# Kernel optimization log

Hardware: AMD Instinct MI355X
Metric: run time of the kernel (lower is better)

Reference implementation:

```python
import jax, jax.numpy as jnp
import numpy as np

S, G, NMUL, LENF = 730, 4000, 2, 15
NEARZERO = 1e-5

# param bounds (change_param_range: lb + raw*(ub-lb)), raw in [0,1]
HBV_LB = np.array([1., 50., .05, .01, .001, .2, 0., 0., -2.5, .5, 0., 0.], np.float32)
HBV_UB = np.array([6., 1000., .9, .5, .2, 1., 10., 100., 2.5, 10., .1, .2], np.float32)
EXP_LB = np.array([0., 100., 10., 0., 0., -3.], np.float32)
EXP_UB = np.array([.1, 1500., 50., 5., 3., 0.], np.float32)


def _descale(raw, lb, ub):
    # raw: [G, n_par, NMUL]
    return lb[None, :, None] + raw * (ub - lb)[None, :, None]


def _hbv(P, T, PET, ph):
    # ph: [G,12,NMUL]; order: beta fc k0 k1 k2 lp perc uzl tt cfmax cfr cwh
    beta, fc, k0, k1, k2, lp, perc, uzl, tt, cfmax, cfr, cwh = [ph[:, i, :] for i in range(12)]

    def step(carry, inp):
        sp, mw, sm, suz, slz = carry
        p, t, pet = inp
        rain = jnp.where(t >= tt, p, 0.)
        sp = sp + jnp.where(t < tt, p, 0.)
        melt = jnp.minimum(jnp.maximum(cfmax * (t - tt), 0.), sp)
        mw = mw + melt; sp = sp - melt
        refr = jnp.minimum(jnp.maximum(cfr * cfmax * (tt - t), 0.), mw)
        sp = sp + refr; mw = mw - refr
        tosoil = jnp.maximum(mw - cwh * sp, 0.)
        mw = mw - tosoil
        sw = jnp.clip((sm / fc) ** beta, 0., 1.)
        rech = (rain + tosoil) * sw
        sm = sm + rain + tosoil - rech
        excess = jnp.maximum(sm - fc, 0.); sm = sm - excess
        et = jnp.minimum(pet * jnp.clip(sm / (lp * fc), 0., 1.), sm)
        sm = jnp.maximum(sm - et, NEARZERO)
        suz = suz + rech + excess
        pa = jnp.minimum(perc, suz); suz = suz - pa
        q0 = k0 * jnp.maximum(suz - uzl, 0.); suz = suz - q0
        q1 = k1 * suz; suz = suz - q1
        slz = slz + pa
        q2 = k2 * slz; slz = slz - q2
        return (sp, mw, sm, suz, slz), q0 + q1 + q2

    z = jnp.full_like(fc, NEARZERO)
    init = (z, z, 0.5 * fc, z, z)
    _, q = jax.lax.scan(step, init, (P, T, PET))
    return q  # [S,G,NMUL]


def _exphydro(P, T, PET, pe):
    # pe: [G,6,NMUL]; order: f smax qmax df tmax tmin
    f, smax, qmax, df, tmax, tmin = [pe[:, i, :] for i in range(6)]

    def step(carry, inp):
        s0, s1 = carry
        p, t, pet = inp
        ps = jnp.where(t <= tmin, p, 0.)
        pr = p - ps
        melt = jnp.where(t > tmax, jnp.minimum(s0, df * (t - tmax)), 0.)
        s0 = s0 + ps - melt
        s1 = s1 + pr + melt
        qspill = jnp.maximum(s1 - smax, 0.); s1 = s1 - qspill
        et = jnp.minimum(pet * jnp.clip(s1 / smax, 0., 1.), s1); s1 = s1 - et
        qb = jnp.minimum(qmax * jnp.exp(-f * jnp.maximum(smax - s1, 0.)), s1)
        s1 = s1 - qb
        return (s0, s1), qspill + qb

    z = jnp.full_like(smax, NEARZERO)
    init = (z, 0.5 * smax)
    _, q = jax.lax.scan(step, init, (P, T, PET))
    return q  # [S,G,NMUL]


def _uh_gamma(a, b):
    # a,b: [G]; gamma-pdf unit hydrograph, lenF=LENF
    aa = jax.nn.relu(a) + 0.1
    th = jax.nn.relu(b) + 0.5
    t = jnp.arange(LENF, dtype=jnp.float32) + 0.5  # [LENF]
    logw = (-jax.scipy.special.gammaln(aa)[None, :] - aa[None, :] * jnp.log(th)[None, :]
            + (aa - 1.)[None, :] * jnp.log(t)[:, None] - t[:, None] / th[None, :])
    w = jnp.exp(logw)
    return w / w.sum(0, keepdims=True)  # [LENF,G]


def _route(q, w):
    # causal depthwise conv: out[t,g] = sum_k w[k,g] * q[t-k,g]
    qp = jnp.pad(q, ((LENF - 1, 0), (0, 0)))
    out = jnp.zeros_like(q)
    for k in range(LENF):
        out = out + w[k][None, :] * qp[LENF - 1 - k: LENF - 1 - k + q.shape[0]]
    return out


def setup_inputs() -> dict:
    key = jax.random.key(0)
    k1, k2 = jax.random.split(key)
    u = jax.random.uniform(k1, (S, G, 3), dtype=jnp.float32)
    # physical forcing ranges: prcp [0,10] mm/d, tmean [-10,20] C, pet [0,5] mm/d
    x = jnp.stack([u[..., 0] * 10., u[..., 1] * 30. - 10., u[..., 2] * 5.], axis=-1)
    raw_phy_static = jax.random.uniform(k2, (G, 18 * NMUL + 2), dtype=jnp.float32)
    return {"x": x, "raw_phy_static": raw_phy_static}


def reference(x, raw_phy_static):
    # unpack: [G, 18*NMUL] static block + 2 routing params
    static = raw_phy_static[:, :18 * NMUL].reshape(G, 18, NMUL)
    ph = _descale(static[:, :12, :], jnp.asarray(HBV_LB), jnp.asarray(HBV_UB))
    pe = _descale(static[:, 12:, :], jnp.asarray(EXP_LB), jnp.asarray(EXP_UB))
    route = raw_phy_static[:, 18 * NMUL:]
    rout_a = route[:, 0] * 2.9   # bounds [0, 2.9]
    rout_b = route[:, 1] * 6.5   # bounds [0, 6.5]

    P = jnp.broadcast_to(x[:, :, 0, None], (S, G, NMUL))
    T = jnp.broadcast_to(x[:, :, 1, None], (S, G, NMUL))
    PET = jnp.broadcast_to(x[:, :, 2, None], (S, G, NMUL))

    q_hbv = _hbv(P, T, PET, ph)
    q_exp = _exphydro(P, T, PET, pe)
    qsim = 0.5 * (q_hbv.mean(-1) + q_exp.mean(-1))  # blend over models, mean over nmul -> [S,G]

    w = _uh_gamma(rout_a, rout_b)
    return _route(qsim, w)  # [S,G] routed streamflow
```

## Files before the change

kernel.cpp:

```cpp
#include <hip/hip_runtime.h>

#define SS 730
#define GG 4000
#define LENF 15
#define PD 10
#define GPAD 4032
#define TT 10
#define QN ((size_t)SS * GG)
#define QNI ((int)(SS * GG))

template<bool STORE4>
__global__ __launch_bounds__(64, 1) void hydro_scan(const float* __restrict__ x,
                                                    const float* __restrict__ raw,
                                                    float* __restrict__ qsim) {
    int tid = blockIdx.x * 64 + threadIdx.x;
    int g = tid % GPAD;
    int inst = tid / GPAD;
    if (g >= GG) return;
    int m = inst & 1;
    const float* pr = raw + (size_t)g * 38 + m;

    int xoff = g * 3;
    int qoff = g + (STORE4 ? inst * QNI : 0);

    float pb[PD], tb[PD], eb[PD];
#pragma unroll
    for (int j = 0; j < PD; ++j) {
        pb[j] = x[xoff]; tb[j] = x[xoff + 1]; eb[j] = x[xoff + 2];
        xoff += 3 * GG;
    }

    if (inst < 2) {
        float beta  = 1.0f   + pr[0]  * 5.0f;
        float fc    = 50.0f  + pr[2]  * 950.0f;
        float k0    = 0.05f  + pr[4]  * 0.85f;
        float k1    = 0.01f  + pr[6]  * 0.49f;
        float k2    = 0.001f + pr[8]  * 0.199f;
        float lp    = 0.2f   + pr[10] * 0.8f;
        float perc  =          pr[12] * 10.0f;
        float uzl   =          pr[14] * 100.0f;
        float tt    = -2.5f  + pr[16] * 5.0f;
        float cfmax = 0.5f   + pr[18] * 9.5f;
        float cfr   =          pr[20] * 0.1f;
        float cwh   =          pr[22] * 0.2f;
        float invfc   = 1.0f / fc;
        float invlpfc = 1.0f / (lp * fc);
        float ncfrcf  = -(cfr * cfmax);
        float omk0    = 1.0f - k0;
        float k0uzl   = k0 * uzl;
        float omk1    = 1.0f - k1;

        float sp = 1e-5f, mw = 1e-5f, sm = 0.5f * fc, suz = 1e-5f, slz = 1e-5f;

        auto body = [&](float p, float tc, float pet) -> float {
            float dt   = tc - tt;
            float msn  = fmaxf(cfmax * dt, 0.0f);
            float mrf  = fmaxf(ncfrcf * dt, 0.0f);
            float rain = (dt >= 0.0f) ? p : 0.0f;
            float snow = p - rain;
            float etk  = fmaf(-invlpfc, pet, 1.0f);
            float sw   = exp2f(beta * __log2f(sm * invfc));
            float omsw = 1.0f - sw;
            float sp1  = sp + snow;
            float melt = fminf(msn, sp1);
            float mw2  = mw + melt;
            float sp2  = sp1 - melt;
            float refr = fminf(mrf, mw2);
            float mw3  = mw2 - refr;
            sp = sp2 + refr;
            float mw4  = fminf(mw3, cwh * sp);
            float tosoil = mw3 - mw4;
            mw = mw4;
            float rt    = rain + tosoil;
            float sm1   = fmaf(rt, omsw, sm);
            float rech  = rt * sw;
            float excess = fmaxf(sm1 - fc, 0.0f);
            float sm2   = fminf(sm1, fc);
            sm = fmaxf(fmaxf(sm2 * etk, sm2 - pet), 1e-5f);
            float suz1 = suz + rech + excess;
            float suz2 = fmaxf(suz1 - perc, 0.0f);
            float pa   = suz1 - suz2;
            float suz3 = fminf(suz2, fmaf(suz2, omk0, k0uzl));
            float suzn = omk1 * suz3;
            float q01  = suz2 - suzn;
            suz = suzn;
            float slz1 = slz + pa;
            float q2   = k2 * slz1;
            slz = slz1 - q2;
            return q01 + q2;
        };

        for (int c = 0; c < SS / PD - 1; ++c) {
#pragma unroll
            for (int j = 0; j < PD; ++j) {
                float p = pb[j], tc = tb[j], pet = eb[j];
                pb[j] = x[xoff]; tb[j] = x[xoff + 1]; eb[j] = x[xoff + 2];
                xoff += 3 * GG;
                float q = body(p, tc, pet);
                if (STORE4) qsim[qoff] = q; else atomicAdd(&qsim[qoff], 0.25f * q);
                qoff += GG;
            }
        }
#pragma unroll
        for (int j = 0; j < PD; ++j) {
            float q = body(pb[j], tb[j], eb[j]);
            if (STORE4) qsim[qoff] = q; else atomicAdd(&qsim[qoff], 0.25f * q);
            qoff += GG;
        }
    } else {
        const float* pe = pr + 24;
        float f    =           pe[0]  * 0.1f;
        float smax = 100.0f  + pe[2]  * 1400.0f;
        float qmax = 10.0f   + pe[4]  * 40.0f;
        float df   =           pe[6]  * 5.0f;
        float tmax =           pe[8]  * 3.0f;
        float tmin = -3.0f   + pe[10] * 3.0f;
        float invsmax = 1.0f / smax;
        float fl = f * 1.44269504f;
        float c0 = __log2f(qmax) - fl * smax;

        float s0 = 1e-5f, s1 = 0.5f * smax;

        auto body = [&](float p, float tc, float pet) -> float {
            float mdf = df * fmaxf(tc - tmax, 0.0f);
            float ps  = (tc <= tmin) ? p : 0.0f;
            float prr = p - ps;
            float etk = fmaxf(fmaf(-invsmax, pet, 1.0f), 0.0f);
            float mlt = fminf(s0, mdf);
            s0 = fmaxf(s0 - mdf, 0.0f) + ps;
            float s1a = s1 + prr + mlt;
            float qspill = fmaxf(s1a - smax, 0.0f);
            float s1b = fminf(s1a, smax);
            float s1c = s1b * etk;
            float qb  = fminf(exp2f(fmaf(fl, s1c, c0)), s1c);
            s1 = s1c - qb;
            return qspill + qb;
        };

        for (int c = 0; c < SS / PD - 1; ++c) {
#pragma unroll
            for (int j = 0; j < PD; ++j) {
                float p = pb[j], tc = tb[j], pet = eb[j];
                pb[j] = x[xoff]; tb[j] = x[xoff + 1]; eb[j] = x[xoff + 2];
                xoff += 3 * GG;
                float q = body(p, tc, pet);
                if (STORE4) qsim[qoff] = q; else atomicAdd(&qsim[qoff], 0.25f * q);
                qoff += GG;
            }
        }
#pragma unroll
        for (int j = 0; j < PD; ++j) {
            float q = body(pb[j], tb[j], eb[j]);
            if (STORE4) qsim[qoff] = q; else atomicAdd(&qsim[qoff], 0.25f * q);
            qoff += GG;
        }
    }
}

__global__ __launch_bounds__(256) void uh_weights(const float* __restrict__ raw,
                                                  float* __restrict__ wbuf) {
    int g = blockIdx.x * 256 + threadIdx.x;
    if (g >= GG) return;
    float a = raw[(size_t)g * 38 + 36] * 2.9f;
    float b = raw[(size_t)g * 38 + 37] * 6.5f;
    float aa = fmaxf(a, 0.0f) + 0.1f;
    float th = fmaxf(b, 0.0f) + 0.5f;
    float am1 = aa - 1.0f;
    float invth = 1.0f / th;

    const float logt[LENF] = {
        -0.69314718f, 0.40546511f, 0.91629073f, 1.25276297f, 1.50407740f,
         1.70474809f, 1.87180218f, 2.01490302f, 2.14006616f, 2.25129180f,
         2.35137526f, 2.44234704f, 2.52572864f, 2.60268969f, 2.67414865f };

    float w[LENF];
    float s = 0.0f;
#pragma unroll
    for (int k = 0; k < LENF; ++k) {
        float tk = (float)k + 0.5f;
        w[k] = expf(am1 * logt[k] - tk * invth);
        s += w[k];
    }
    float scale = 0.25f / s;
#pragma unroll
    for (int k = 0; k < LENF; ++k)
        wbuf[(size_t)k * GG + g] = w[k] * scale;
}

template<int NB, bool WPRE>
__global__ __launch_bounds__(256) void hydro_route(const float* __restrict__ qsim,
                                                   const float* __restrict__ raw,
                                                   const float* __restrict__ wbuf,
                                                   float* __restrict__ out) {
    int idx = blockIdx.x * 256 + threadIdx.x;
    if (idx >= GG * (SS / TT)) return;
    int g = idx % GG;
    int c = idx / GG;
    int t0 = c * TT;

    float w[LENF];
    float scale;
    if (WPRE) {
#pragma unroll
        for (int k = 0; k < LENF; ++k)
            w[k] = wbuf[(size_t)k * GG + g];
        scale = 1.0f;
    } else {
        float a = raw[(size_t)g * 38 + 36] * 2.9f;
        float b = raw[(size_t)g * 38 + 37] * 6.5f;
        float aa = fmaxf(a, 0.0f) + 0.1f;
        float th = fmaxf(b, 0.0f) + 0.5f;
        float am1 = aa - 1.0f;
        float invth = 1.0f / th;
        const float logt[LENF] = {
            -0.69314718f, 0.40546511f, 0.91629073f, 1.25276297f, 1.50407740f,
             1.70474809f, 1.87180218f, 2.01490302f, 2.14006616f, 2.25129180f,
             2.35137526f, 2.44234704f, 2.52572864f, 2.60268969f, 2.67414865f };
        float s = 0.0f;
#pragma unroll
        for (int k = 0; k < LENF; ++k) {
            float tk = (float)k + 0.5f;
            w[k] = expf(am1 * logt[k] - tk * invth);
            s += w[k];
        }
        scale = (NB == 4 ? 0.25f : 1.0f) / s;
    }

    float v[TT + LENF - 1];
#pragma unroll
    for (int i = 0; i < TT + LENF - 1; ++i) {
        int tp = t0 - (LENF - 1) + i;
        float sv = 0.0f;
        if (tp >= 0) {
            const float* qb = qsim + (size_t)tp * GG + g;
            sv = qb[0];
            if (NB == 4) sv += qb[QN] + qb[2 * QN] + qb[3 * QN];
        }
        v[i] = sv;
    }
#pragma unroll
    for (int j = 0; j < TT; ++j) {
        float acc = 0.0f;
#pragma unroll
        for (int k = 0; k < LENF; ++k)
            acc += w[k] * v[j + (LENF - 1) - k];
        out[(size_t)(t0 + j) * GG + g] = (WPRE ? acc : acc * scale);
    }
}

extern "C" void kernel_launch(void* const* d_in, const int* in_sizes, int n_in,
                              void* d_out, int out_size, void* d_ws, size_t ws_size,
                              hipStream_t stream) {
    const float* x   = (const float*)d_in[0];
    const float* raw = (const float*)d_in[1];
    float* out  = (float*)d_out;
    float* qsim = (float*)d_ws;

    const size_t slices4 = 4 * QN * sizeof(float);
    const size_t wbytes  = (size_t)LENF * GG * sizeof(float);
    int rblocks = (GG * (SS / TT) + 255) / 256;

    if (ws_size >= slices4 + wbytes) {
        float* wbuf = qsim + 4 * QN;
        hydro_scan<true><<<(4 * GPAD) / 64, 64, 0, stream>>>(x, raw, qsim);
        uh_weights<<<(GG + 255) / 256, 256, 0, stream>>>(raw, wbuf);
        hydro_route<4, true><<<rblocks, 256, 0, stream>>>(qsim, raw, wbuf, out);
    } else if (ws_size >= slices4) {
        hydro_scan<true><<<(4 * GPAD) / 64, 64, 0, stream>>>(x, raw, qsim);
        hydro_route<4, false><<<rblocks, 256, 0, stream>>>(qsim, raw, nullptr, out);
    } else {
        hipMemsetAsync(qsim, 0, QN * sizeof(float), stream);
        hydro_scan<false><<<(4 * GPAD) / 64, 64, 0, stream>>>(x, raw, qsim);
        hydro_route<1, false><<<rblocks, 256, 0, stream>>>(qsim, raw, nullptr, out);
    }
}
```

Baseline: 111.2 us.

## Software-pipeline HBV and ExpHydro recurrences across timesteps to shorten dependency chains

Splits each timestep of both the HBV and ExpHydro scan bodies into stages (snow, soil, response) and skews them across consecutive timesteps. The soil-wetness power term for the next step is computed right after the soil update, so its log/exp latency overlaps with independent work from other stages. The goal is to break the serial latency chain in this latency-bound, one-wave-per-block recurrence. The cost is extra prologue and epilogue code and more live registers, and the launcher drops the middle workspace-size branch.

```diff
diff --git a/kernel.cpp b/kernel.cpp
--- a/kernel.cpp
+++ b/kernel.cpp
@@ -51,16 +51,18 @@
         float omk1    = 1.0f - k1;
 
         float sp = 1e-5f, mw = 1e-5f, sm = 0.5f * fc, suz = 1e-5f, slz = 1e-5f;
-
-        auto body = [&](float p, float tc, float pet) -> float {
+        float swc = exp2f(beta * __log2f(sm * invfc));
+        float rech = 0.0f, exc = 0.0f;
+        float rech_b = 0.0f, exc_b = 0.0f;
+        float rt_p = 0.0f, pet_p = 0.0f;
+        float qprev = 0.0f;
+
+        auto S1 = [&](float p, float tc) -> float {
             float dt   = tc - tt;
             float msn  = fmaxf(cfmax * dt, 0.0f);
             float mrf  = fmaxf(ncfrcf * dt, 0.0f);
             float rain = (dt >= 0.0f) ? p : 0.0f;
             float snow = p - rain;
-            float etk  = fmaf(-invlpfc, pet, 1.0f);
-            float sw   = exp2f(beta * __log2f(sm * invfc));
-            float omsw = 1.0f - sw;
             float sp1  = sp + snow;
             float melt = fminf(msn, sp1);
             float mw2  = mw + melt;
@@ -71,13 +73,20 @@
             float mw4  = fminf(mw3, cwh * sp);
             float tosoil = mw3 - mw4;
             mw = mw4;
-            float rt    = rain + tosoil;
-            float sm1   = fmaf(rt, omsw, sm);
-            float rech  = rt * sw;
-            float excess = fmaxf(sm1 - fc, 0.0f);
-            float sm2   = fminf(sm1, fc);
+            return rain + tosoil;
+        };
+        auto S2 = [&](float rt, float pet) {
+            float omsw = 1.0f - swc;
+            float sm1  = fmaf(rt, omsw, sm);
+            rech = rt * swc;
+            exc  = fmaxf(sm1 - fc, 0.0f);
+            float sm2  = fminf(sm1, fc);
+            float etk  = fmaf(-invlpfc, pet, 1.0f);
             sm = fmaxf(fmaxf(sm2 * etk, sm2 - pet), 1e-5f);
-            float suz1 = suz + rech + excess;
+            swc = exp2f(beta * __log2f(sm * invfc));
+        };
+        auto S3 = [&](float rb, float ebx) -> float {
+            float suz1 = suz + rb + ebx;
             float suz2 = fmaxf(suz1 - perc, 0.0f);
             float pa   = suz1 - suz2;
             float suz3 = fminf(suz2, fmaf(suz2, omk0, k0uzl));
@@ -89,24 +98,57 @@
             slz = slz1 - q2;
             return q01 + q2;
         };
-
-        for (int c = 0; c < SS / PD - 1; ++c) {
-#pragma unroll
-            for (int j = 0; j < PD; ++j) {
-                float p = pb[j], tc = tb[j], pet = eb[j];
+        auto full = [&](int j, bool pre, bool st) {
+            if (st) {
+                if (STORE4) qsim[qoff] = qprev;
+                else atomicAdd(&qsim[qoff], 0.25f * qprev);
+                qoff += GG;
+            }
+            float p = pb[j], tc = tb[j], pet = eb[j];
+            if (pre) {
                 pb[j] = x[xoff]; tb[j] = x[xoff + 1]; eb[j] = x[xoff + 2];
                 xoff += 3 * GG;
-                float q = body(p, tc, pet);
-                if (STORE4) qsim[qoff] = q; else atomicAdd(&qsim[qoff], 0.25f * q);
-                qoff += GG;
             }
-        }
-#pragma unroll
-        for (int j = 0; j < PD; ++j) {
-            float q = body(pb[j], tb[j], eb[j]);
-            if (STORE4) qsim[qoff] = q; else atomicAdd(&qsim[qoff], 0.25f * q);
-            qoff += GG;
-        }
+            float qv = S3(rech_b, exc_b);
+            S2(rt_p, pet_p);
+            float rt = S1(p, tc);
+            rech_b = rech; exc_b = exc;
+            rt_p = rt; pet_p = pet;
+            qprev = qv;
+        };
+
+        {
+            float p = pb[0], tc = tb[0], pet = eb[0];
+            pb[0] = x[xoff]; tb[0] = x[xoff + 1]; eb[0] = x[xoff + 2];
+            xoff += 3 * GG;
+            rt_p = S1(p, tc); pet_p = pet;
+        }
+        {
+            float p = pb[1], tc = tb[1], pet = eb[1];
+            pb[1] = x[xoff]; tb[1] = x[xoff + 1]; eb[1] = x[xoff + 2];
+            xoff += 3 * GG;
+            S2(rt_p, pet_p);
+            rech_b = rech; exc_b = exc;
+            rt_p = S1(p, tc); pet_p = pet;
+        }
+        full(2, true, false);
+#pragma unroll
+        for (int j = 3; j < PD; ++j) full(j, true, true);
+        for (int c = 1; c < SS / PD - 1; ++c) {
+#pragma unroll
+            for (int j = 0; j < PD; ++j) full(j, true, true);
+        }
+#pragma unroll
+        for (int j = 0; j < PD; ++j) full(j, false, true);
+        if (STORE4) { qsim[qoff] = qprev; qoff += GG; }
+        else { atomicAdd(&qsim[qoff], 0.25f * qprev); qoff += GG; }
+        S2(rt_p, pet_p);
+        float qv = S3(rech_b, exc_b);
+        if (STORE4) { qsim[qoff] = qv; qoff += GG; }
+        else { atomicAdd(&qsim[qoff], 0.25f * qv); qoff += GG; }
+        float qf = S3(rech, exc);
+        if (STORE4) qsim[qoff] = qf;
+        else atomicAdd(&qsim[qoff], 0.25f * qf);
     } else {
         const float* pe = pr + 24;
         float f    =           pe[0]  * 0.1f;
@@ -120,14 +162,19 @@
         float c0 = __log2f(qmax) - fl * smax;
 
         float s0 = 1e-5f, s1 = 0.5f * smax;
-
-        auto body = [&](float p, float tc, float pet) -> float {
+        float prr_p = 0.0f, mlt_p = 0.0f, pet_p = 0.0f;
+        float qprev = 0.0f;
+
+        auto S1e = [&](float p, float tc) {
             float mdf = df * fmaxf(tc - tmax, 0.0f);
             float ps  = (tc <= tmin) ? p : 0.0f;
             float prr = p - ps;
-            float etk = fmaxf(fmaf(-invsmax, pet, 1.0f), 0.0f);
             float mlt = fminf(s0, mdf);
             s0 = fmaxf(s0 - mdf, 0.0f) + ps;
+            prr_p = prr; mlt_p = mlt;
+        };
+        auto S2e = [&](float prr, float mlt, float pet) -> float {
+            float etk = fmaxf(fmaf(-invsmax, pet, 1.0f), 0.0f);
             float s1a = s1 + prr + mlt;
             float qspill = fmaxf(s1a - smax, 0.0f);
             float s1b = fminf(s1a, smax);
@@ -136,24 +183,44 @@
             s1 = s1c - qb;
             return qspill + qb;
         };
-
-        for (int c = 0; c < SS / PD - 1; ++c) {
-#pragma unroll
-            for (int j = 0; j < PD; ++j) {
-                float p = pb[j], tc = tb[j], pet = eb[j];
+        auto full = [&](int j, bool pre, bool st) {
+            if (st) {
+                if (STORE4) qsim[qoff] = qprev;
+                else atomicAdd(&qsim[qoff], 0.25f * qprev);
+                qoff += GG;
+            }
+            float p = pb[j], tc = tb[j], pet = eb[j];
+            if (pre) {
                 pb[j] = x[xoff]; tb[j] = x[xoff + 1]; eb[j] = x[xoff + 2];
                 xoff += 3 * GG;
-                float q = body(p, tc, pet);
-                if (STORE4) qsim[qoff] = q; else atomicAdd(&qsim[qoff], 0.25f * q);
-                qoff += GG;
             }
-        }
-#pragma unroll
-        for (int j = 0; j < PD; ++j) {
-            float q = body(pb[j], tb[j], eb[j]);
-            if (STORE4) qsim[qoff] = q; else atomicAdd(&qsim[qoff], 0.25f * q);
-            qoff += GG;
-        }
+            float prr = prr_p, mlt = mlt_p, peto = pet_p;
+            S1e(p, tc);
+            float qv = S2e(prr, mlt, peto);
+            pet_p = pet;
+            qprev = qv;
+        };
+
+        {
+            float p = pb[0], tc = tb[0], pet = eb[0];
+            pb[0] = x[xoff]; tb[0] = x[xoff + 1]; eb[0] = x[xoff + 2];
+            xoff += 3 * GG;
+            S1e(p, tc); pet_p = pet;
+        }
+        full(1, true, false);
+#pragma unroll
+        for (int j = 2; j < PD; ++j) full(j, true, true);
+        for (int c = 1; c < SS / PD - 1; ++c) {
+#pragma unroll
+            for (int j = 0; j < PD; ++j) full(j, true, true);
+        }
+#pragma unroll
+        for (int j = 0; j < PD; ++j) full(j, false, true);
+        if (STORE4) { qsim[qoff] = qprev; qoff += GG; }
+        else { atomicAdd(&qsim[qoff], 0.25f * qprev); qoff += GG; }
+        float qf = S2e(prr_p, mlt_p, pet_p);
+        if (STORE4) qsim[qoff] = qf;
+        else atomicAdd(&qsim[qoff], 0.25f * qf);
     }
 }
 
@@ -259,18 +326,16 @@
     const size_t slices4 = 4 * QN * sizeof(float);
     const size_t wbytes  = (size_t)LENF * GG * sizeof(float);
     int rblocks = (GG * (SS / TT) + 255) / 256;
+    int sblocks = (4 * GPAD) / 64;
 
     if (ws_size >= slices4 + wbytes) {
         float* wbuf = qsim + 4 * QN;
-        hydro_scan<true><<<(4 * GPAD) / 64, 64, 0, stream>>>(x, raw, qsim);
+        hydro_scan<true><<<sblocks, 64, 0, stream>>>(x, raw, qsim);
         uh_weights<<<(GG + 255) / 256, 256, 0, stream>>>(raw, wbuf);
         hydro_route<4, true><<<rblocks, 256, 0, stream>>>(qsim, raw, wbuf, out);
-    } else if (ws_size >= slices4) {
-        hydro_scan<true><<<(4 * GPAD) / 64, 64, 0, stream>>>(x, raw, qsim);
-        hydro_route<4, false><<<rblocks, 256, 0, stream>>>(qsim, raw, nullptr, out);
     } else {
         hipMemsetAsync(qsim, 0, QN * sizeof(float), stream);
-        hydro_scan<false><<<(4 * GPAD) / 64, 64, 0, stream>>>(x, raw, qsim);
+        hydro_scan<false><<<sblocks, 64, 0, stream>>>(x, raw, qsim);
         hydro_route<1, false><<<rblocks, 256, 0, stream>>>(qsim, raw, nullptr, out);
     }
 }
```

Measured after the change: 123.4 us. +11.0%, slower.

## Pack both NMUL members per thread using float2 vectors, halving scan threads

Applied to the files above, without the earlier changes.

Each scan thread now handles both NMUL parameter sets of one model through 2-wide float vectors, so the scan launches 2*GPAD threads instead of 4*GPAD. The two members are summed in-thread, which halves the qsim intermediate slices written and read by the routing kernel. It also reuses the same x loads for both members. In exchange, each thread has a longer dependency chain and uses more registers, and parallelism drops to about 8000 threads, which could leave many compute units idle on a latency-bound recurrence.

```diff
diff --git a/kernel.cpp b/kernel.cpp
--- a/kernel.cpp
+++ b/kernel.cpp
@@ -9,19 +9,35 @@
 #define QN ((size_t)SS * GG)
 #define QNI ((int)(SS * GG))
 
-template<bool STORE4>
+typedef float v2 __attribute__((ext_vector_type(2)));
+static __device__ __forceinline__ v2 vmin(v2 a, v2 b) {
+    v2 r; r.x = fminf(a.x, b.x); r.y = fminf(a.y, b.y); return r;
+}
+static __device__ __forceinline__ v2 vmax(v2 a, v2 b) {
+    v2 r; r.x = fmaxf(a.x, b.x); r.y = fmaxf(a.y, b.y); return r;
+}
+static __device__ __forceinline__ v2 vmax0(v2 a) {
+    v2 r; r.x = fmaxf(a.x, 0.0f); r.y = fmaxf(a.y, 0.0f); return r;
+}
+static __device__ __forceinline__ v2 vexp2(v2 a) {
+    v2 r; r.x = exp2f(a.x); r.y = exp2f(a.y); return r;
+}
+static __device__ __forceinline__ v2 vlog2(v2 a) {
+    v2 r; r.x = __log2f(a.x); r.y = __log2f(a.y); return r;
+}
+
+template<bool STORE2>
 __global__ __launch_bounds__(64, 1) void hydro_scan(const float* __restrict__ x,
                                                     const float* __restrict__ raw,
                                                     float* __restrict__ qsim) {
     int tid = blockIdx.x * 64 + threadIdx.x;
     int g = tid % GPAD;
-    int inst = tid / GPAD;
+    int model = tid / GPAD;
     if (g >= GG) return;
-    int m = inst & 1;
-    const float* pr = raw + (size_t)g * 38 + m;
+    const v2* prv = reinterpret_cast<const v2*>(raw + (size_t)g * 38);
 
     int xoff = g * 3;
-    int qoff = g + (STORE4 ? inst * QNI : 0);
+    int qoff = g + (STORE2 ? model * QNI : 0);
 
     float pb[PD], tb[PD], eb[PD];
 #pragma unroll
@@ -30,64 +46,69 @@
         xoff += 3 * GG;
     }
 
-    if (inst < 2) {
-        float beta  = 1.0f   + pr[0]  * 5.0f;
-        float fc    = 50.0f  + pr[2]  * 950.0f;
-        float k0    = 0.05f  + pr[4]  * 0.85f;
-        float k1    = 0.01f  + pr[6]  * 0.49f;
-        float k2    = 0.001f + pr[8]  * 0.199f;
-        float lp    = 0.2f   + pr[10] * 0.8f;
-        float perc  =          pr[12] * 10.0f;
-        float uzl   =          pr[14] * 100.0f;
-        float tt    = -2.5f  + pr[16] * 5.0f;
-        float cfmax = 0.5f   + pr[18] * 9.5f;
-        float cfr   =          pr[20] * 0.1f;
-        float cwh   =          pr[22] * 0.2f;
-        float invfc   = 1.0f / fc;
-        float invlpfc = 1.0f / (lp * fc);
-        float ncfrcf  = -(cfr * cfmax);
-        float omk0    = 1.0f - k0;
-        float k0uzl   = k0 * uzl;
-        float omk1    = 1.0f - k1;
-
-        float sp = 1e-5f, mw = 1e-5f, sm = 0.5f * fc, suz = 1e-5f, slz = 1e-5f;
+    if (model == 0) {
+        v2 beta  = 1.0f   + prv[0]  * 5.0f;
+        v2 fc    = 50.0f  + prv[1]  * 950.0f;
+        v2 k0    = 0.05f  + prv[2]  * 0.85f;
+        v2 k1    = 0.01f  + prv[3]  * 0.49f;
+        v2 k2    = 0.001f + prv[4]  * 0.199f;
+        v2 lp    = 0.2f   + prv[5]  * 0.8f;
+        v2 perc  =          prv[6]  * 10.0f;
+        v2 uzl   =          prv[7]  * 100.0f;
+        v2 tt    = -2.5f  + prv[8]  * 5.0f;
+        v2 cfmax = 0.5f   + prv[9]  * 9.5f;
+        v2 cfr   =          prv[10] * 0.1f;
+        v2 cwh   =          prv[11] * 0.2f;
+        v2 invfc;   invfc.x = 1.0f / fc.x;  invfc.y = 1.0f / fc.y;
+        v2 invlpfc; invlpfc.x = 1.0f / (lp.x * fc.x); invlpfc.y = 1.0f / (lp.y * fc.y);
+        v2 ncfrcf = -(cfr * cfmax);
+        v2 omk0   = 1.0f - k0;
+        v2 k0uzl  = k0 * uzl;
+        v2 omk1   = 1.0f - k1;
+
+        v2 sp = {1e-5f, 1e-5f}, mw = {1e-5f, 1e-5f};
+        v2 sm = 0.5f * fc;
+        v2 suz = {1e-5f, 1e-5f}, slz = {1e-5f, 1e-5f};
 
         auto body = [&](float p, float tc, float pet) -> float {
-            float dt   = tc - tt;
-            float msn  = fmaxf(cfmax * dt, 0.0f);
-            float mrf  = fmaxf(ncfrcf * dt, 0.0f);
-            float rain = (dt >= 0.0f) ? p : 0.0f;
-            float snow = p - rain;
-            float etk  = fmaf(-invlpfc, pet, 1.0f);
-            float sw   = exp2f(beta * __log2f(sm * invfc));
-            float omsw = 1.0f - sw;
-            float sp1  = sp + snow;
-            float melt = fminf(msn, sp1);
-            float mw2  = mw + melt;
-            float sp2  = sp1 - melt;
-            float refr = fminf(mrf, mw2);
-            float mw3  = mw2 - refr;
+            v2 dt   = tc - tt;
+            v2 msn  = vmax0(cfmax * dt);
+            v2 mrf  = vmax0(ncfrcf * dt);
+            v2 rain; rain.x = (dt.x >= 0.0f) ? p : 0.0f;
+                     rain.y = (dt.y >= 0.0f) ? p : 0.0f;
+            v2 snow = p - rain;
+            v2 etk  = 1.0f - invlpfc * pet;
+            v2 sw   = vexp2(beta * vlog2(sm * invfc));
+            v2 omsw = 1.0f - sw;
+            v2 sp1  = sp + snow;
+            v2 melt = vmin(msn, sp1);
+            v2 mw2  = mw + melt;
+            v2 sp2  = sp1 - melt;
+            v2 refr = vmin(mrf, mw2);
+            v2 mw3  = mw2 - refr;
             sp = sp2 + refr;
-            float mw4  = fminf(mw3, cwh * sp);
-            float tosoil = mw3 - mw4;
+            v2 mw4  = vmin(mw3, cwh * sp);
+            v2 tosoil = mw3 - mw4;
             mw = mw4;
-            float rt    = rain + tosoil;
-            float sm1   = fmaf(rt, omsw, sm);
-            float rech  = rt * sw;
-            float excess = fmaxf(sm1 - fc, 0.0f);
-            float sm2   = fminf(sm1, fc);
-            sm = fmaxf(fmaxf(sm2 * etk, sm2 - pet), 1e-5f);
-            float suz1 = suz + rech + excess;
-            float suz2 = fmaxf(suz1 - perc, 0.0f);
-            float pa   = suz1 - suz2;
-            float suz3 = fminf(suz2, fmaf(suz2, omk0, k0uzl));
-            float suzn = omk1 * suz3;
-            float q01  = suz2 - suzn;
+            v2 rt     = rain + tosoil;
+            v2 sm1    = sm + rt * omsw;
+            v2 rech   = rt * sw;
+            v2 excess = vmax0(sm1 - fc);
+            v2 sm2    = vmin(sm1, fc);
+            v2 smlo   = {1e-5f, 1e-5f};
+            sm = vmax(vmax(sm2 * etk, sm2 - pet), smlo);
+            v2 suz1 = suz + rech + excess;
+            v2 suz2 = vmax0(suz1 - perc);
+            v2 pa   = suz1 - suz2;
+            v2 suz3 = vmin(suz2, suz2 * omk0 + k0uzl);
+            v2 suzn = omk1 * suz3;
+            v2 q01  = suz2 - suzn;
             suz = suzn;
-            float slz1 = slz + pa;
-            float q2   = k2 * slz1;
+            v2 slz1 = slz + pa;
+            v2 q2   = k2 * slz1;
             slz = slz1 - q2;
-            return q01 + q2;
+            v2 q = q01 + q2;
+            return q.x + q.y;
         };
 
         for (int c = 0; c < SS / PD - 1; ++c) {
@@ -97,44 +118,47 @@
                 pb[j] = x[xoff]; tb[j] = x[xoff + 1]; eb[j] = x[xoff + 2];
                 xoff += 3 * GG;
                 float q = body(p, tc, pet);
-                if (STORE4) qsim[qoff] = q; else atomicAdd(&qsim[qoff], 0.25f * q);
+                if (STORE2) qsim[qoff] = q; else atomicAdd(&qsim[qoff], 0.25f * q);
                 qoff += GG;
             }
         }
 #pragma unroll
         for (int j = 0; j < PD; ++j) {
             float q = body(pb[j], tb[j], eb[j]);
-            if (STORE4) qsim[qoff] = q; else atomicAdd(&qsim[qoff], 0.25f * q);
+            if (STORE2) qsim[qoff] = q; else atomicAdd(&qsim[qoff], 0.25f * q);
             qoff += GG;
         }
     } else {
-        const float* pe = pr + 24;
-        float f    =           pe[0]  * 0.1f;
-        float smax = 100.0f  + pe[2]  * 1400.0f;
-        float qmax = 10.0f   + pe[4]  * 40.0f;
-        float df   =           pe[6]  * 5.0f;
-        float tmax =           pe[8]  * 3.0f;
-        float tmin = -3.0f   + pe[10] * 3.0f;
-        float invsmax = 1.0f / smax;
-        float fl = f * 1.44269504f;
-        float c0 = __log2f(qmax) - fl * smax;
-
-        float s0 = 1e-5f, s1 = 0.5f * smax;
+        v2 f    =           prv[12] * 0.1f;
+        v2 smax = 100.0f  + prv[13] * 1400.0f;
+        v2 qmax = 10.0f   + prv[14] * 40.0f;
+        v2 df   =           prv[15] * 5.0f;
+        v2 tmax =           prv[16] * 3.0f;
+        v2 tmin = -3.0f   + prv[17] * 3.0f;
+        v2 invsmax; invsmax.x = 1.0f / smax.x; invsmax.y = 1.0f / smax.y;
+        v2 fl = f * 1.44269504f;
+        v2 c0; c0.x = __log2f(qmax.x) - fl.x * smax.x;
+               c0.y = __log2f(qmax.y) - fl.y * smax.y;
+
+        v2 s0 = {1e-5f, 1e-5f};
+        v2 s1 = 0.5f * smax;
 
         auto body = [&](float p, float tc, float pet) -> float {
-            float mdf = df * fmaxf(tc - tmax, 0.0f);
-            float ps  = (tc <= tmin) ? p : 0.0f;
-            float prr = p - ps;
-            float etk = fmaxf(fmaf(-invsmax, pet, 1.0f), 0.0f);
-            float mlt = fminf(s0, mdf);
-            s0 = fmaxf(s0 - mdf, 0.0f) + ps;
-            float s1a = s1 + prr + mlt;
-            float qspill = fmaxf(s1a - smax, 0.0f);
-            float s1b = fminf(s1a, smax);
-            float s1c = s1b * etk;
-            float qb  = fminf(exp2f(fmaf(fl, s1c, c0)), s1c);
+            v2 mdf = df * vmax0(tc - tmax);
+            v2 ps; ps.x = (tc <= tmin.x) ? p : 0.0f;
+                   ps.y = (tc <= tmin.y) ? p : 0.0f;
+            v2 prr = p - ps;
+            v2 etk = vmax0(1.0f - invsmax * pet);
+            v2 mlt = vmin(s0, mdf);
+            s0 = vmax0(s0 - mdf) + ps;
+            v2 s1a = s1 + prr + mlt;
+            v2 qspill = vmax0(s1a - smax);
+            v2 s1b = vmin(s1a, smax);
+            v2 s1c = s1b * etk;
+            v2 qb  = vmin(vexp2(fl * s1c + c0), s1c);
             s1 = s1c - qb;
-            return qspill + qb;
+            v2 q = qspill + qb;
+            return q.x + q.y;
         };
 
         for (int c = 0; c < SS / PD - 1; ++c) {
@@ -144,14 +168,14 @@
                 pb[j] = x[xoff]; tb[j] = x[xoff + 1]; eb[j] = x[xoff + 2];
                 xoff += 3 * GG;
                 float q = body(p, tc, pet);
-                if (STORE4) qsim[qoff] = q; else atomicAdd(&qsim[qoff], 0.25f * q);
+                if (STORE2) qsim[qoff] = q; else atomicAdd(&qsim[qoff], 0.25f * q);
                 qoff += GG;
             }
         }
 #pragma unroll
         for (int j = 0; j < PD; ++j) {
             float q = body(pb[j], tb[j], eb[j]);
-            if (STORE4) qsim[qoff] = q; else atomicAdd(&qsim[qoff], 0.25f * q);
+            if (STORE2) qsim[qoff] = q; else atomicAdd(&qsim[qoff], 0.25f * q);
             qoff += GG;
         }
     }
@@ -223,7 +247,7 @@
             w[k] = expf(am1 * logt[k] - tk * invth);
             s += w[k];
         }
-        scale = (NB == 4 ? 0.25f : 1.0f) / s;
+        scale = (NB == 2 ? 0.25f : 1.0f) / s;
     }
 
     float v[TT + LENF - 1];
@@ -234,7 +258,7 @@
         if (tp >= 0) {
             const float* qb = qsim + (size_t)tp * GG + g;
             sv = qb[0];
-            if (NB == 4) sv += qb[QN] + qb[2 * QN] + qb[3 * QN];
+            if (NB == 2) sv += qb[QN];
         }
         v[i] = sv;
     }
@@ -256,21 +280,19 @@
     float* out  = (float*)d_out;
     float* qsim = (float*)d_ws;
 
-    const size_t slices4 = 4 * QN * sizeof(float);
+    const size_t slices2 = 2 * QN * sizeof(float);
     const size_t wbytes  = (size_t)LENF * GG * sizeof(float);
     int rblocks = (GG * (SS / TT) + 255) / 256;
-
-    if (ws_size >= slices4 + wbytes) {
-        float* wbuf = qsim + 4 * QN;
-        hydro_scan<true><<<(4 * GPAD) / 64, 64, 0, stream>>>(x, raw, qsim);
+    int sblocks = (2 * GPAD) / 64;
+
+    if (ws_size >= slices2 + wbytes) {
+        float* wbuf = qsim + 2 * QN;
+        hydro_scan<true><<<sblocks, 64, 0, stream>>>(x, raw, qsim);
         uh_weights<<<(GG + 255) / 256, 256, 0, stream>>>(raw, wbuf);
-        hydro_route<4, true><<<rblocks, 256, 0, stream>>>(qsim, raw, wbuf, out);
-    } else if (ws_size >= slices4) {
-        hydro_scan<true><<<(4 * GPAD) / 64, 64, 0, stream>>>(x, raw, qsim);
-        hydro_route<4, false><<<rblocks, 256, 0, stream>>>(qsim, raw, nullptr, out);
+        hydro_route<2, true><<<rblocks, 256, 0, stream>>>(qsim, raw, wbuf, out);
     } else {
         hipMemsetAsync(qsim, 0, QN * sizeof(float), stream);
-        hydro_scan<false><<<(4 * GPAD) / 64, 64, 0, stream>>>(x, raw, qsim);
+        hydro_scan<false><<<sblocks, 64, 0, stream>>>(x, raw, qsim);
         hydro_route<1, false><<<rblocks, 256, 0, stream>>>(qsim, raw, nullptr, out);
     }
 }
```

Result: slower. 144.3 us (+29.8%).
